# Optimization experiments

Hardware: AMD Instinct MI355X
Metric: run time of the kernel (lower is better)

## Reference

```python
import jax, jax.numpy as jnp
import numpy as np
from jax import lax

BAD = -10000.0
K = 10
W = 512  # window_size


def setup_inputs() -> dict:
    key = jax.random.key(0)
    k1, k2, k3, k4 = jax.random.split(key, 4)
    S, B, P, D, R = 4, 256, 32768, 256, 1000
    return {
        "relation": jax.random.randint(k1, (S, B), 0, R, dtype=jnp.int32),
        "head": jax.random.randint(k2, (S, B), 0, P, dtype=jnp.int32),
        "entity_embedding": jax.random.normal(k3, (S, P, D), dtype=jnp.float32),
        "relation_embedding": jax.random.normal(k4, (R, D), dtype=jnp.float32),
    }


def reference(relation, head, entity_embedding, relation_embedding):
    S, B = relation.shape
    P, D = entity_embedding.shape[1], entity_embedding.shape[2]
    Q = S * B            # total queries after all_gather
    NBEST = K + 1
    n_rep = -(-P // W)   # ceil

    # all_gather of queries across shards (every shard sees all queries)
    rel_all = relation.reshape(-1)                                   # (Q,)
    head_emb_all = entity_embedding[jnp.arange(S)[:, None], head]    # (S,B,D)
    head_emb_all = head_emb_all.reshape(Q, D)
    # DistMult score_tails: <h, r, t> ; fold h*r into one query vector
    qvec = head_emb_all * relation_embedding[rel_all]                # (Q,D)

    init_sc = jnp.full((S, Q, NBEST), BAD, dtype=jnp.float32)
    init_ix = jnp.full((S, Q, NBEST), P, dtype=jnp.int32)

    def step(carry, w):
        sc, ix = carry
        start = w * W
        # local idx of this window, clamped like the torch mask branch
        raw = start + jnp.arange(W, dtype=jnp.int32)                 # (W,)
        valid = raw < P
        slide = jnp.where(valid, raw, P - 1)
        neg = lax.dynamic_slice_in_dim(entity_embedding,
                                       jnp.minimum(start, P - W), W, axis=1)  # (S,W,D)
        scores_w = jnp.einsum('qd,swd->sqw', qvec, neg)              # (S,Q,W)
        scores_w = scores_w + BAD * (~valid).astype(scores_w.dtype)
        all_sc = jnp.concatenate([scores_w, sc], axis=-1)            # (S,Q,W+NBEST)
        all_ix = jnp.concatenate(
            [jnp.broadcast_to(slide, (S, Q, W)), ix], axis=-1)
        top_sc, top_pos = lax.top_k(all_sc, NBEST)
        top_ix = jnp.take_along_axis(all_ix, top_pos, axis=-1)
        return (top_sc, top_ix), None

    (best_sc, best_ix), _ = lax.scan(step, (init_sc, init_ix),
                                     jnp.arange(n_rep, dtype=jnp.int32))

    # all_to_all: (src_shard, dst_shard, bs, nbest) -> (dst, src, bs, nbest)
    best_sc = best_sc.reshape(S, S, B, NBEST).transpose(1, 0, 2, 3)
    best_ix = best_ix.reshape(S, S, B, NBEST).transpose(1, 0, 2, 3)

    # mask out placeholder / padding local indices (shard_counts == P)
    best_sc = best_sc + BAD * (best_ix >= P).astype(best_sc.dtype)

    # shard_and_idx_to_entity: interleaved global ids, padded column for idx==P
    base = jnp.arange(P, dtype=jnp.int32)[None, :] * S \
        + jnp.arange(S, dtype=jnp.int32)[:, None]                    # (S,P)
    table = jnp.concatenate(
        [base, jnp.full((S, 1), -1, dtype=jnp.int32)], axis=1)       # (S,P+1)
    src = jnp.arange(S, dtype=jnp.int32)[None, :, None, None]
    best_gid = table[src, best_ix]                                   # (S,S,B,NBEST)

    # per destination shard: merge the S per-source-shard top-(k+1) lists
    sc_flat = best_sc.transpose(0, 2, 1, 3).reshape(S, B, S * NBEST)
    gid_flat = best_gid.transpose(0, 2, 1, 3).reshape(S, B, S * NBEST)
    topk_sc, topk_pos = lax.top_k(sc_flat, K)                        # (S,B,K)
    topk_gid = jnp.take_along_axis(gid_flat, topk_pos, axis=-1)
    return topk_gid, topk_sc
```

## Files before the change

kernel.cpp:

```cpp
#include <hip/hip_runtime.h>

#define SS 4
#define BB 256
#define PP 32768
#define DD 256
#define QQ 1024
#define NN 131072
#define KTOP 10
#define QTILE 128
#define WQ 32
#define NCHUNK 64
#define CHROWS 2048
#define PANEL 64
#define NPANEL (CHROWS / PANEL)
#define JCH 8
#define MSLOT 20
#define ROWG 33
#define ROWE (ROWG * 8)
#define PANB (PANEL * ROWG * 16)
#define KEYMASK 0xFFFFF800u
#define MWS 132
#define CVB 4096

typedef __attribute__((ext_vector_type(8))) short bf16x8;
typedef __attribute__((ext_vector_type(4))) short s16x4;
typedef __attribute__((ext_vector_type(4))) float f32x4;
typedef __attribute__((ext_vector_type(16))) float f32x16;
typedef __attribute__((ext_vector_type(4))) unsigned int u32x4;

static __device__ __forceinline__ short f2bf(float f) {
    union { float f; unsigned u; } v; v.f = f;
    unsigned r = (v.u + 0x7FFFu + ((v.u >> 16) & 1u)) >> 16;
    return (short)r;
}
static __device__ __forceinline__ unsigned umax(unsigned a, unsigned b) { return a > b ? a : b; }
static __device__ __forceinline__ unsigned med3u(unsigned k, unsigned a, unsigned b) {
    unsigned d;
    asm("v_med3_u32 %0, %1, %2, %3" : "=v"(d) : "v"(k), "v"(a), "v"(b));
    return d;
}

__global__ void prep_kernel(const int* __restrict__ rel, const int* __restrict__ head,
                            const float* __restrict__ E, const float* __restrict__ R,
                            short* __restrict__ Ebf, short* __restrict__ qbf) {
    if (blockIdx.x < CVB) {
        size_t base = (size_t)blockIdx.x * 8192;
        #pragma unroll
        for (int c = 0; c < 8; c++) {
            size_t idx = base + (size_t)c * 1024 + (size_t)threadIdx.x * 4;
            f32x4 a = *(const f32x4*)(E + idx);
            s16x4 o;
            o[0] = f2bf(a[0]); o[1] = f2bf(a[1]); o[2] = f2bf(a[2]); o[3] = f2bf(a[3]);
            *(s16x4*)(Ebf + idx) = o;
        }
    } else {
        int q = blockIdx.x - CVB, d = threadIdx.x;
        int s1 = q >> 8;
        float f = E[((size_t)(s1 * PP + head[q])) * DD + d] * R[(size_t)rel[q] * DD + d];
        qbf[q * DD + d] = f2bf(f);
    }
}

__launch_bounds__(256, 2)
__global__ void score_topk_kernel(const short* __restrict__ Ebf, const short* __restrict__ qbf,
                                  unsigned* __restrict__ parts) {
    __shared__ __align__(16) char smem[2 * PANB];

    const int tid  = threadIdx.x;
    const int wave = tid >> 6;
    const int lane = tid & 63;
    const int lh   = lane >> 5;
    const int ln   = lane & 31;
    const int mtile = blockIdx.x >> 6;
    const int chunk = blockIdx.x & 63;

    short* buf0 = (short*)smem;
    short* buf1 = (short*)(smem + PANB);

    bf16x8 afrag[16];
    {
        const int arow = mtile * QTILE + wave * WQ + ln;
        #pragma unroll
        for (int ks = 0; ks < 16; ks++)
            afrag[ks] = *(const bf16x8*)(qbf + arow * DD + ks * 16 + lh * 8);
    }

    unsigned lst[16][4];
    #pragma unroll
    for (int r = 0; r < 16; r++)
        #pragma unroll
        for (int i = 0; i < 4; i++) lst[r][i] = 0u;

    const int n0c = chunk * CHROWS;

    bf16x8 st[8];
    #pragma unroll
    for (int it = 0; it < 8; it++) {
        int gi = it * 256 + tid, row = gi >> 5, slot = gi & 31;
        st[it] = *(const bf16x8*)(Ebf + (size_t)(n0c + row) * DD + slot * 8);
    }
    #pragma unroll
    for (int it = 0; it < 8; it++) {
        int gi = it * 256 + tid, row = gi >> 5, slot = gi & 31;
        *(bf16x8*)(buf0 + row * ROWE + slot * 8) = st[it];
    }

    for (int p = 0; p < NPANEL; p++) {
        short* bp = (p & 1) ? buf1 : buf0;
        short* bn = (p & 1) ? buf0 : buf1;
        __syncthreads();
        if (p + 1 < NPANEL) {
            const int n1 = n0c + (p + 1) * PANEL;
            #pragma unroll
            for (int it = 0; it < 8; it++) {
                int gi = it * 256 + tid, row = gi >> 5, slot = gi & 31;
                st[it] = *(const bf16x8*)(Ebf + (size_t)(n1 + row) * DD + slot * 8);
            }
        }

        f32x16 acc0, acc1;
        #pragma unroll
        for (int r = 0; r < 16; r++) { acc0[r] = 256.0f; acc1[r] = 256.0f; }
        const short* b0 = bp + ln * ROWE + lh * 8;
        const short* b1 = bp + (32 + ln) * ROWE + lh * 8;
        #pragma unroll
        for (int ks = 0; ks < 16; ks++) {
            bf16x8 x0 = *(const bf16x8*)(b0 + ks * 16);
            bf16x8 x1 = *(const bf16x8*)(b1 + ks * 16);
            acc0 = __builtin_amdgcn_mfma_f32_32x32x16_bf16(afrag[ks], x0, acc0, 0, 0, 0);
            acc1 = __builtin_amdgcn_mfma_f32_32x32x16_bf16(afrag[ks], x1, acc1, 0, 0, 0);
        }

        const unsigned c0 = (unsigned)(p * 64 + ln);
        const unsigned c1 = (unsigned)(p * 64 + 32 + ln);
        #pragma unroll
        for (int r = 0; r < 16; r++) {
            unsigned key = (__float_as_uint(acc0[r]) & KEYMASK) | c0;
            unsigned n0 = med3u(key, lst[r][0], lst[r][1]);
            unsigned n1 = med3u(key, lst[r][1], lst[r][2]);
            unsigned n2 = med3u(key, lst[r][2], lst[r][3]);
            lst[r][3] = umax(key, lst[r][3]);
            lst[r][0] = n0; lst[r][1] = n1; lst[r][2] = n2;
        }
        #pragma unroll
        for (int r = 0; r < 16; r++) {
            unsigned key = (__float_as_uint(acc1[r]) & KEYMASK) | c1;
            unsigned n0 = med3u(key, lst[r][0], lst[r][1]);
            unsigned n1 = med3u(key, lst[r][1], lst[r][2]);
            unsigned n2 = med3u(key, lst[r][2], lst[r][3]);
            lst[r][3] = umax(key, lst[r][3]);
            lst[r][0] = n0; lst[r][1] = n1; lst[r][2] = n2;
        }

        if (p + 1 < NPANEL) {
            #pragma unroll
            for (int it = 0; it < 8; it++) {
                int gi = it * 256 + tid, row = gi >> 5, slot = gi & 31;
                *(bf16x8*)(bn + row * ROWE + slot * 8) = st[it];
            }
        }
    }

    __syncthreads();
    unsigned* mw = (unsigned*)smem + (size_t)wave * (WQ * MWS);
    #pragma unroll
    for (int r = 0; r < 16; r++) {
        int q = (r & 3) + 8 * (r >> 2) + 4 * lh;
        u32x4 v; v[0] = lst[r][0]; v[1] = lst[r][1]; v[2] = lst[r][2]; v[3] = lst[r][3];
        *(u32x4*)(mw + q * MWS + ln * 4) = v;
    }
    if (lane < 32) {
        unsigned rr[JCH];
        #pragma unroll
        for (int i = 0; i < JCH; i++) rr[i] = 0u;
        #pragma unroll
        for (int j = 0; j < 32; j++) {
            u32x4 v = *(const u32x4*)(mw + lane * MWS + j * 4);
            #pragma unroll
            for (int e = 0; e < 4; e++) {
                unsigned x = v[e];
                unsigned t0 = med3u(x, rr[0], rr[1]);
                unsigned t1 = med3u(x, rr[1], rr[2]);
                unsigned t2 = med3u(x, rr[2], rr[3]);
                unsigned t3 = med3u(x, rr[3], rr[4]);
                unsigned t4 = med3u(x, rr[4], rr[5]);
                unsigned t5 = med3u(x, rr[5], rr[6]);
                unsigned t6 = med3u(x, rr[6], rr[7]);
                rr[7] = umax(x, rr[7]);
                rr[0]=t0; rr[1]=t1; rr[2]=t2; rr[3]=t3; rr[4]=t4; rr[5]=t5; rr[6]=t6;
            }
        }
        const int qg = mtile * QTILE + wave * WQ + lane;
        unsigned* dst = parts + ((size_t)qg * NCHUNK + chunk) * JCH;
        #pragma unroll
        for (int i = 0; i < JCH; i++) dst[i] = rr[JCH - 1 - i];
    }
}

__global__ void finalize_kernel(const int* __restrict__ rel, const int* __restrict__ head,
                                const float* __restrict__ E, const float* __restrict__ R,
                                const unsigned* __restrict__ parts, float* __restrict__ out) {
    __shared__ float qv[DD];
    __shared__ int   gl[MSLOT];
    __shared__ float rsc[MSLOT];
    __shared__ int   rgid[MSLOT];

    const int q = blockIdx.x;
    const int tid = threadIdx.x;
    const int wave = tid >> 6, lane = tid & 63;
    const int s1 = q >> 8;

    qv[tid] = E[((size_t)(s1 * PP + head[q])) * DD + tid] * R[(size_t)rel[q] * DD + tid];

    if (wave == 0) {
        unsigned run[JCH];
        const unsigned* src = parts + ((size_t)q * NCHUNK + lane) * JCH;
        #pragma unroll
        for (int j = 0; j < JCH; j++) run[j] = src[j];
        for (int r = 0; r < MSLOT; r++) {
            unsigned best = run[0]; int bl = lane;
            #pragma unroll
            for (int off = 32; off >= 1; off >>= 1) {
                unsigned ob = __shfl_xor(best, off);
                int ol = __shfl_xor(bl, off);
                if (ob > best || (ob == best && ol < bl)) { best = ob; bl = ol; }
            }
            if (lane == bl) {
                int col = (int)(best & 0x7FFu);
                int n = lane * CHROWS + col;
                gl[r] = ((n & (PP - 1)) << 2) | (n >> 15);
                #pragma unroll
                for (int j = 0; j < JCH - 1; j++) run[j] = run[j + 1];
                run[JCH - 1] = 0u;
            }
        }
    }
    __syncthreads();

    f32x4 qq = *(const f32x4*)(qv + lane * 4);
    #pragma unroll
    for (int c = 0; c < MSLOT / 4; c++) {
        int j = wave * (MSLOT / 4) + c;
        int gid = gl[j];
        int n = (gid & 3) * PP + (gid >> 2);
        f32x4 ev = *(const f32x4*)(E + (size_t)n * DD + lane * 4);
        f32x4 p = qq * ev;
        float s = (p[0] + p[1]) + (p[2] + p[3]);
        #pragma unroll
        for (int off = 32; off >= 1; off >>= 1) s += __shfl_xor(s, off);
        if (lane == 0) { rsc[j] = s; rgid[j] = gid; }
    }
    __syncthreads();

    if (tid < 64) {
        float a = (tid < MSLOT) ? rsc[tid] : -1e30f;
        int   g = (tid < MSLOT) ? rgid[tid] : 0;
        for (int r = 0; r < KTOP; r++) {
            float ps = a; int pg = g; int plm = tid;
            #pragma unroll
            for (int off = 32; off >= 1; off >>= 1) {
                float os = __shfl_xor(ps, off);
                int   og = __shfl_xor(pg, off);
                int   ol = __shfl_xor(plm, off);
                if (os > ps || (os == ps && ol < plm)) { ps = os; pg = og; plm = ol; }
            }
            if (tid == 0) {
                out[q * KTOP + r]             = (float)pg;
                out[QQ * KTOP + q * KTOP + r] = ps;
            }
            if (tid == plm) a = -1e30f;
        }
    }
}

extern "C" void kernel_launch(void* const* d_in, const int* in_sizes, int n_in,
                              void* d_out, int out_size, void* d_ws, size_t ws_size,
                              hipStream_t stream) {
    const int*   rel  = (const int*)d_in[0];
    const int*   head = (const int*)d_in[1];
    const float* E    = (const float*)d_in[2];
    const float* R    = (const float*)d_in[3];

    char* ws = (char*)d_ws;
    short* Ebf = (short*)ws;
    short* qbf = (short*)(ws + (size_t)NN * DD * 2);
    unsigned* parts = (unsigned*)(ws + (size_t)NN * DD * 2 + (size_t)QQ * DD * 2);

    prep_kernel<<<dim3(CVB + QQ), dim3(256), 0, stream>>>(rel, head, E, R, Ebf, qbf);
    score_topk_kernel<<<dim3((QQ / QTILE) * NCHUNK), dim3(256), 0, stream>>>(Ebf, qbf, parts);
    finalize_kernel<<<dim3(QQ), dim3(256), 0, stream>>>(rel, head, E, R, parts, (float*)d_out);
}
```

Measured before the change: 297.1 us.

## Fuse fp32-to-bf16 entity conversion into the scoring kernel's tile loads

Drops the separate pass that turns the whole entity table into bf16 in workspace. The scoring kernel now reads fp32 rows straight from the input and packs them to bf16 with v_cvt_pk_bf16_f32 while staging each panel into shared memory. This removes one full read and write of the table, but each of the 8 query tiles now reads the fp32 source, doubling bytes per panel load, and the conversion ALU work is repeated across tiles. The rounding mode of the hardware convert may also differ from the manual one.

```diff
diff --git a/kernel.cpp b/kernel.cpp
--- a/kernel.cpp
+++ b/kernel.cpp
@@ -20,10 +20,8 @@
 #define PANB (PANEL * ROWG * 16)
 #define KEYMASK 0xFFFFF800u
 #define MWS 132
-#define CVB 4096
 
 typedef __attribute__((ext_vector_type(8))) short bf16x8;
-typedef __attribute__((ext_vector_type(4))) short s16x4;
 typedef __attribute__((ext_vector_type(4))) float f32x4;
 typedef __attribute__((ext_vector_type(16))) float f32x16;
 typedef __attribute__((ext_vector_type(4))) unsigned int u32x4;
@@ -39,30 +37,29 @@
     asm("v_med3_u32 %0, %1, %2, %3" : "=v"(d) : "v"(k), "v"(a), "v"(b));
     return d;
 }
+static __device__ __forceinline__ unsigned pkbf(float lo, float hi) {
+    unsigned d;
+    asm("v_cvt_pk_bf16_f32 %0, %1, %2" : "=v"(d) : "v"(lo), "v"(hi));
+    return d;
+}
+static __device__ __forceinline__ bf16x8 cvt8pk(f32x4 a, f32x4 b) {
+    union { u32x4 u; bf16x8 h; } c;
+    c.u[0] = pkbf(a[0], a[1]); c.u[1] = pkbf(a[2], a[3]);
+    c.u[2] = pkbf(b[0], b[1]); c.u[3] = pkbf(b[2], b[3]);
+    return c.h;
+}
 
 __global__ void prep_kernel(const int* __restrict__ rel, const int* __restrict__ head,
                             const float* __restrict__ E, const float* __restrict__ R,
-                            short* __restrict__ Ebf, short* __restrict__ qbf) {
-    if (blockIdx.x < CVB) {
-        size_t base = (size_t)blockIdx.x * 8192;
-        #pragma unroll
-        for (int c = 0; c < 8; c++) {
-            size_t idx = base + (size_t)c * 1024 + (size_t)threadIdx.x * 4;
-            f32x4 a = *(const f32x4*)(E + idx);
-            s16x4 o;
-            o[0] = f2bf(a[0]); o[1] = f2bf(a[1]); o[2] = f2bf(a[2]); o[3] = f2bf(a[3]);
-            *(s16x4*)(Ebf + idx) = o;
-        }
-    } else {
-        int q = blockIdx.x - CVB, d = threadIdx.x;
-        int s1 = q >> 8;
-        float f = E[((size_t)(s1 * PP + head[q])) * DD + d] * R[(size_t)rel[q] * DD + d];
-        qbf[q * DD + d] = f2bf(f);
-    }
+                            short* __restrict__ qbf) {
+    int q = blockIdx.x, d = threadIdx.x;
+    int s1 = q >> 8;
+    float f = E[((size_t)(s1 * PP + head[q])) * DD + d] * R[(size_t)rel[q] * DD + d];
+    qbf[q * DD + d] = f2bf(f);
 }
 
 __launch_bounds__(256, 2)
-__global__ void score_topk_kernel(const short* __restrict__ Ebf, const short* __restrict__ qbf,
+__global__ void score_topk_kernel(const float* __restrict__ E, const short* __restrict__ qbf,
                                   unsigned* __restrict__ parts) {
     __shared__ __align__(16) char smem[2 * PANB];
 
@@ -92,18 +89,19 @@
         for (int i = 0; i < 4; i++) lst[r][i] = 0u;
 
     const int n0c = chunk * CHROWS;
+    const int srow = tid >> 5, sslot = tid & 31;
 
     bf16x8 st[8];
     #pragma unroll
     for (int it = 0; it < 8; it++) {
-        int gi = it * 256 + tid, row = gi >> 5, slot = gi & 31;
-        st[it] = *(const bf16x8*)(Ebf + (size_t)(n0c + row) * DD + slot * 8);
-    }
-    #pragma unroll
-    for (int it = 0; it < 8; it++) {
-        int gi = it * 256 + tid, row = gi >> 5, slot = gi & 31;
-        *(bf16x8*)(buf0 + row * ROWE + slot * 8) = st[it];
-    }
+        const float* src = E + (size_t)(n0c + it * 8 + srow) * DD + sslot * 8;
+        f32x4 a = *(const f32x4*)src;
+        f32x4 b = *(const f32x4*)(src + 4);
+        st[it] = cvt8pk(a, b);
+    }
+    #pragma unroll
+    for (int it = 0; it < 8; it++)
+        *(bf16x8*)(buf0 + (it * 8 + srow) * ROWE + sslot * 8) = st[it];
 
     for (int p = 0; p < NPANEL; p++) {
         short* bp = (p & 1) ? buf1 : buf0;
@@ -113,8 +111,10 @@
             const int n1 = n0c + (p + 1) * PANEL;
             #pragma unroll
             for (int it = 0; it < 8; it++) {
-                int gi = it * 256 + tid, row = gi >> 5, slot = gi & 31;
-                st[it] = *(const bf16x8*)(Ebf + (size_t)(n1 + row) * DD + slot * 8);
+                const float* src = E + (size_t)(n1 + it * 8 + srow) * DD + sslot * 8;
+                f32x4 a = *(const f32x4*)src;
+                f32x4 b = *(const f32x4*)(src + 4);
+                st[it] = cvt8pk(a, b);
             }
         }
 
@@ -154,10 +154,8 @@
 
         if (p + 1 < NPANEL) {
             #pragma unroll
-            for (int it = 0; it < 8; it++) {
-                int gi = it * 256 + tid, row = gi >> 5, slot = gi & 31;
-                *(bf16x8*)(bn + row * ROWE + slot * 8) = st[it];
-            }
+            for (int it = 0; it < 8; it++)
+                *(bf16x8*)(bn + (it * 8 + srow) * ROWE + sslot * 8) = st[it];
         }
     }
 
@@ -282,11 +280,10 @@
     const float* R    = (const float*)d_in[3];
 
     char* ws = (char*)d_ws;
-    short* Ebf = (short*)ws;
-    short* qbf = (short*)(ws + (size_t)NN * DD * 2);
-    unsigned* parts = (unsigned*)(ws + (size_t)NN * DD * 2 + (size_t)QQ * DD * 2);
-
-    prep_kernel<<<dim3(CVB + QQ), dim3(256), 0, stream>>>(rel, head, E, R, Ebf, qbf);
-    score_topk_kernel<<<dim3((QQ / QTILE) * NCHUNK), dim3(256), 0, stream>>>(Ebf, qbf, parts);
+    short* qbf = (short*)ws;
+    unsigned* parts = (unsigned*)(ws + (size_t)QQ * DD * 2);
+
+    prep_kernel<<<dim3(QQ), dim3(256), 0, stream>>>(rel, head, E, R, qbf);
+    score_topk_kernel<<<dim3((QQ / QTILE) * NCHUNK), dim3(256), 0, stream>>>(E, qbf, parts);
     finalize_kernel<<<dim3(QQ), dim3(256), 0, stream>>>(rel, head, E, R, parts, (float*)d_out);
 }
```

Measured after the change: 315.3 us. 6.1% more time.
